# Kernel tuning notes

Hardware: AMD Instinct MI355X
Metric: run time of the kernel (lower is better)

The kernel has to match this reference:

```python
import jax, jax.numpy as jnp
import numpy as np

NOISE_EPS = 1e-2


def setup_inputs() -> dict:
    key = jax.random.key(0)
    ks = jax.random.split(key, 6)
    N, D, E, H = 16384, 512, 8, 1024
    x = jax.random.normal(ks[0], (N, D), jnp.float32)
    eps = jax.random.normal(ks[1], (N, E), jnp.float32)
    w_gate = jax.random.normal(ks[2], (D, E), jnp.float32) * 0.02
    w_noise = jax.random.normal(ks[3], (D, E), jnp.float32) * 0.02
    W_h = jnp.eye(E, dtype=jnp.float32)  # module initializes W_h = eye(num_experts)
    W1 = jax.random.normal(ks[4], (E, D, H), jnp.float32) * 0.02
    b1 = jnp.zeros((E, H), jnp.float32)
    W2 = jax.random.normal(ks[5], (E, H, D), jnp.float32) * 0.02
    b2 = jnp.zeros((E, D), jnp.float32)
    return dict(x=x, eps=eps, w_gate=w_gate, w_noise=w_noise, W_h=W_h,
                W1=W1, b1=b1, W2=W2, b2=b2, k=2, capacity=5120)


def reference(x, eps, w_gate, w_noise, W_h, W1, b1, W2, b2, k, capacity):
    N, D = x.shape
    E = w_gate.shape[1]
    # --- noisy top-k gating ---
    clean_logits = (x @ w_gate) @ W_h                       # [N, E]
    noise_stddev = jax.nn.softplus(x @ w_noise) + NOISE_EPS  # [N, E]
    noisy_logits = clean_logits + eps * noise_stddev
    top_vals, top_idx = jax.lax.top_k(noisy_logits, k)       # [N, k]
    top_gates = jax.nn.softmax(top_vals, axis=-1)
    gates = jnp.zeros((N, E), x.dtype).at[jnp.arange(N)[:, None], top_idx].set(top_gates)
    # --- capacity masking: keep the first `capacity` routed tokens per expert (batch order) ---
    active = gates > 0
    rank = jnp.cumsum(active, axis=0) - 1                    # per-expert arrival rank
    keep = active & (rank < capacity)
    gates = jnp.where(keep, gates, jnp.zeros((), x.dtype))
    # --- dispatch into fixed [E, capacity] buffers (dummy slot absorbs dropped writes) ---
    flat = jnp.where(keep, jnp.arange(E)[None, :] * capacity + rank, E * capacity)  # [N, E]
    tok = jnp.broadcast_to(jnp.arange(N, dtype=jnp.int32)[:, None], (N, E))
    buf = jnp.zeros(E * capacity + 1, jnp.int32).at[flat].set(tok)[:E * capacity].reshape(E, capacity)
    gbuf = jnp.zeros(E * capacity + 1, x.dtype).at[flat].set(gates)[:E * capacity].reshape(E, capacity)
    x_exp = x[buf]                                           # [E, C, D] gather
    # --- per-expert 1-layer FFN (grouped GEMM) ---
    h = jax.nn.relu(jnp.einsum('ecd,edh->ech', x_exp, W1) + b1[:, None, :])
    y_exp = jnp.einsum('ech,eho->eco', h, W2) + b2[:, None, :]
    # --- weighted scatter-combine (unfilled slots have gate 0, so they add nothing) ---
    weighted = y_exp * gbuf[..., None]
    combined = jnp.zeros((N, D), x.dtype).at[buf.reshape(-1)].add(weighted.reshape(-1, D))
    return combined
```

## Files before the change

kernel.cpp:

```cpp
#include <hip/hip_runtime.h>
#include <hip/hip_bf16.h>
#include <cstdint>

#define NTOK 16384
#define DIM 512
#define NEXP 8
#define HID 1024
#define CAPACITY 5120

typedef __attribute__((ext_vector_type(8))) short bf16x8;
typedef __attribute__((ext_vector_type(4))) float f32x4;
typedef unsigned long long u64;

__device__ __forceinline__ unsigned short f2bf(float f) {
    unsigned u = __float_as_uint(f);
    unsigned r = (u + 0x7FFFu + ((u >> 16) & 1u)) >> 16;
    return (unsigned short)r;
}

#define GLDS16(gp, lp) __builtin_amdgcn_global_load_lds( \
    (const __attribute__((address_space(1))) void*)(gp), \
    (__attribute__((address_space(3))) void*)(lp), 16, 0, 0)

__global__ __launch_bounds__(256) void gating_kernel(
    const float* __restrict__ x, const float* __restrict__ eps,
    const float* __restrict__ wg, const float* __restrict__ wn,
    const float* __restrict__ Wh, int2* __restrict__ rec)
{
    int w = threadIdx.x >> 6, lane = threadIdx.x & 63;
    int n = blockIdx.x * 4 + w;
    float ag[8], an[8];
#pragma unroll
    for (int e = 0; e < 8; ++e) { ag[e] = 0.f; an[e] = 0.f; }
    const float* xr = x + (size_t)n * DIM;
#pragma unroll
    for (int i = 0; i < DIM / 64; ++i) {
        int d = i * 64 + lane;
        float xv = xr[d];
        const float4* g4 = reinterpret_cast<const float4*>(wg + (size_t)d * 8);
        const float4* n4 = reinterpret_cast<const float4*>(wn + (size_t)d * 8);
        float4 a0 = g4[0], a1 = g4[1], b0 = n4[0], b1v = n4[1];
        ag[0] += xv * a0.x; ag[1] += xv * a0.y; ag[2] += xv * a0.z; ag[3] += xv * a0.w;
        ag[4] += xv * a1.x; ag[5] += xv * a1.y; ag[6] += xv * a1.z; ag[7] += xv * a1.w;
        an[0] += xv * b0.x; an[1] += xv * b0.y; an[2] += xv * b0.z; an[3] += xv * b0.w;
        an[4] += xv * b1v.x; an[5] += xv * b1v.y; an[6] += xv * b1v.z; an[7] += xv * b1v.w;
    }
#pragma unroll
    for (int off = 32; off; off >>= 1) {
#pragma unroll
        for (int e = 0; e < 8; ++e) {
            ag[e] += __shfl_xor(ag[e], off);
            an[e] += __shfl_xor(an[e], off);
        }
    }
    float noisy[8];
#pragma unroll
    for (int e = 0; e < 8; ++e) {
        float c = 0.f;
#pragma unroll
        for (int j = 0; j < 8; ++j) c += ag[j] * Wh[j * 8 + e];
        float v = an[e];
        float sp = fmaxf(v, 0.f) + log1pf(expf(-fabsf(v)));
        noisy[e] = c + eps[(size_t)n * 8 + e] * (sp + 1e-2f);
    }
    int i1 = 0; float v1 = noisy[0];
#pragma unroll
    for (int e = 1; e < 8; ++e) if (noisy[e] > v1) { v1 = noisy[e]; i1 = e; }
    int i2 = -1; float v2 = -3.4e38f;
#pragma unroll
    for (int e = 0; e < 8; ++e) if (e != i1 && noisy[e] > v2) { v2 = noisy[e]; i2 = e; }
    float ex = expf(v2 - v1);
    float g1 = 1.f / (1.f + ex);
    if (lane == 0)
        rec[n] = make_int2(i1 | (i2 << 8), __float_as_int(g1));
}

__global__ __launch_bounds__(1024) void scan_local(
    const int2* __restrict__ rec, unsigned* __restrict__ lrank, int* __restrict__ btot)
{
    __shared__ u64 wtot[16];
    __shared__ int wprefix[16][8];
    int tid = threadIdx.x, w = tid >> 6, lane = tid & 63;
    int n = blockIdx.x * 1024 + tid;
    int2 r = rec[n];
    int e1 = r.x & 0xFF, e2 = (r.x >> 8) & 0xFF;
    u64 m = (1ULL << (e1 * 8)) | (1ULL << (e2 * 8));
    u64 incl = m;
#pragma unroll
    for (int off = 1; off < 64; off <<= 1) {
        u64 v = __shfl_up(incl, off);
        if (lane >= off) incl += v;
    }
    if (lane == 63) wtot[w] = incl;
    __syncthreads();
    if (tid < 128) {
        int e = tid & 7, ww = tid >> 3;
        int s = 0;
        for (int j = 0; j < ww; ++j) s += (int)((wtot[j] >> (e * 8)) & 0xFF);
        wprefix[ww][e] = s;
        if (ww == 15)
            btot[blockIdx.x * 8 + e] = s + (int)((wtot[15] >> (e * 8)) & 0xFF);
    }
    __syncthreads();
    u64 excl = incl - m;
    unsigned l1 = (unsigned)(wprefix[w][e1] + (int)((excl >> (e1 * 8)) & 0xFF));
    unsigned l2 = (unsigned)(wprefix[w][e2] + (int)((excl >> (e2 * 8)) & 0xFF));
    lrank[n] = l1 | (l2 << 16);
}

__global__ __launch_bounds__(64) void scan_offs(
    const int* __restrict__ btot, int* __restrict__ off, int* __restrict__ counts,
    const int* __restrict__ cap_p)
{
    int e = threadIdx.x;
    if (e >= 8) return;
    int cap = *cap_p; if (cap > CAPACITY) cap = CAPACITY;
    int run = 0;
    for (int b = 0; b < 16; ++b) {
        off[b * 8 + e] = run;
        run += btot[b * 8 + e];
    }
    counts[e] = min(run, cap);
}

__global__ __launch_bounds__(1024) void scatter_k(
    const int2* __restrict__ rec, const unsigned* __restrict__ lrank,
    const int* __restrict__ off, const int* __restrict__ cap_p,
    int* __restrict__ buf, float* __restrict__ gbuf)
{
    int tid = threadIdx.x, b = blockIdx.x;
    int n = b * 1024 + tid;
    int cap = *cap_p; if (cap > CAPACITY) cap = CAPACITY;
    int2 r = rec[n];
    int e1 = r.x & 0xFF, e2 = (r.x >> 8) & 0xFF;
    float g1 = __int_as_float(r.y), g2 = 1.f - g1;
    unsigned lr = lrank[n];
    int r1 = off[b * 8 + e1] + (int)(lr & 0xFFFF);
    int r2 = off[b * 8 + e2] + (int)(lr >> 16);
    if (r1 < cap) { buf[e1 * CAPACITY + r1] = n; gbuf[e1 * CAPACITY + r1] = g1; }
    if (r2 < cap) { buf[e2 * CAPACITY + r2] = n; gbuf[e2 * CAPACITY + r2] = g2; }
}

__global__ __launch_bounds__(256) void gather_x(
    const float* __restrict__ x, const int* __restrict__ buf,
    const int* __restrict__ counts, unsigned short* __restrict__ xe)
{
    int slot = blockIdx.x * 4 + (threadIdx.x >> 6);
    int lane = threadIdx.x & 63;
    int e = slot / CAPACITY, rr = slot - e * CAPACITY;
    int4 v = make_int4(0, 0, 0, 0);
    if (rr < counts[e]) {
        int tok = buf[slot];
        const float* src = x + (size_t)tok * DIM + lane * 8;
        float4 a = *reinterpret_cast<const float4*>(src);
        float4 b = *reinterpret_cast<const float4*>(src + 4);
        v.x = f2bf(a.x) | ((int)f2bf(a.y) << 16);
        v.y = f2bf(a.z) | ((int)f2bf(a.w) << 16);
        v.z = f2bf(b.x) | ((int)f2bf(b.y) << 16);
        v.w = f2bf(b.z) | ((int)f2bf(b.w) << 16);
    }
    *reinterpret_cast<int4*>(xe + (size_t)e * CAPACITY * DIM +
                             ((size_t)lane * CAPACITY + rr) * 8) = v;
}

__global__ __launch_bounds__(256) void tcvt(const float* __restrict__ in,
                                            unsigned short* __restrict__ out, int R, int C)
{
    __shared__ float tile[32][33];
    int z = blockIdx.z;
    int c0 = blockIdx.x * 32, r0 = blockIdx.y * 32;
    int tx = threadIdx.x, ty = threadIdx.y;
    const float* inz = in + (size_t)z * R * C;
    unsigned short* outz = out + (size_t)z * R * C;
#pragma unroll
    for (int j = 0; j < 32; j += 8)
        tile[ty + j][tx] = inz[(size_t)(r0 + ty + j) * C + c0 + tx];
    __syncthreads();
#pragma unroll
    for (int j = 0; j < 32; j += 8)
        outz[(size_t)(c0 + ty + j) * R + r0 + tx] = f2bf(tile[tx][ty + j]);
}


#define STAGEB(T, BI)                                                      \
  {                                                                        \
    size_t k0_ = (size_t)(T) * 64;                                         \
    char* db_ = lds + (BI) * 16384 + w * 4096 + lane * 16;                 \
    GLDS16(Bt + boff[0] + k0_, db_);                                       \
    GLDS16(Bt + boff[1] + k0_, db_ + 1024);                                \
    GLDS16(Bt + boff[2] + k0_, db_ + 2048);                                \
    GLDS16(Bt + boff[3] + k0_, db_ + 3072);                                \
  }

#define LOADA(T, AF)                                                       \
  {                                                                        \
    const unsigned short* ab_ = A + abase + (size_t)(T) * (CAPACITY * 64); \
    _Pragma("unroll")                                                      \
    for (int kk = 0; kk < 2; ++kk)                                         \
      _Pragma("unroll")                                                    \
      for (int mi = 0; mi < 4; ++mi)                                       \
        AF[kk][mi] = *reinterpret_cast<const bf16x8*>(ab_ + voff[kk][mi]); \
  }

#define COMPUTE(BI, AF)                                                    \
  {                                                                        \
    const char* cb_ = lds + (BI) * 16384;                                  \
    _Pragma("unroll")                                                      \
    for (int kk = 0; kk < 2; ++kk) {                                       \
      bf16x8 bfr_[4];                                                      \
      _Pragma("unroll")                                                    \
      for (int ni = 0; ni < 4; ++ni) {                                     \
        int row_ = wn * 64 + ni * 16 + rl;                                 \
        int cc_ = (kk * 4 + q) ^ (row_ & 7);                               \
        bfr_[ni] = *reinterpret_cast<const bf16x8*>(cb_ + row_ * 128 + cc_ * 16); \
      }                                                                    \
      _Pragma("unroll")                                                    \
      for (int mi = 0; mi < 4; ++mi)                                       \
        _Pragma("unroll")                                                  \
        for (int ni = 0; ni < 4; ++ni)                                     \
          acc[mi][ni] = __builtin_amdgcn_mfma_f32_16x16x32_bf16(           \
              AF[kk][mi], bfr_[ni], acc[mi][ni], 0, 0, 0);                 \
    }                                                                      \
  }

#define VMCNT12 asm volatile("s_waitcnt vmcnt(12)" ::: "memory")
#define BARRIER asm volatile("s_barrier" ::: "memory")

template <int MODE>
__global__ __launch_bounds__(256) void ffn_gemm(
    const unsigned short* __restrict__ A, const unsigned short* __restrict__ Bt,
    const float* __restrict__ bias, unsigned short* __restrict__ Hout,
    float* __restrict__ Out, const int* __restrict__ buf,
    const float* __restrict__ gbuf, const int* __restrict__ counts,
    int Ka, int Nd)
{
    int flat = blockIdx.x + gridDim.x * (blockIdx.y + gridDim.y * blockIdx.z);
    int e  = flat & 7;
    int rr = flat >> 3;
    int tn = rr % gridDim.y;
    int tm = rr / gridDim.y;

    int cnt = counts[e];
    if (tm * 128 >= cnt) return;
    int tid = threadIdx.x, w = tid >> 6, lane = tid & 63;
    int q = lane >> 4, rl = lane & 15;
    int wm = w >> 1, wn = w & 1;

    __shared__ __align__(16) char lds[32768];

    unsigned boff[4];
#pragma unroll
    for (int i = 0; i < 4; ++i) {
        int p = (w * 4 + i) * 64 + lane;
        int row = p >> 3, kp = p & 7;
        int c = kp ^ (row & 7);
        boff[i] = (unsigned)(e * Nd + tn * 128 + row) * Ka + c * 8;
    }

    size_t abase = (size_t)e * CAPACITY * Ka;
    unsigned voff[2][4];
#pragma unroll
    for (int kk = 0; kk < 2; ++kk)
#pragma unroll
        for (int mi = 0; mi < 4; ++mi) {
            int row = tm * 128 + wm * 64 + mi * 16 + rl;
            voff[kk][mi] = (unsigned)((kk * 4 + q) * CAPACITY + row) * 8;
        }

    f32x4 acc[4][4];
#pragma unroll
    for (int mi = 0; mi < 4; ++mi)
#pragma unroll
        for (int ni = 0; ni < 4; ++ni)
            acc[mi][ni] = (f32x4){0.f, 0.f, 0.f, 0.f};

    int nk = Ka >> 6;

    bf16x8 afA[2][4], afB[2][4];

    STAGEB(0, 0);
    LOADA(0, afA);

    for (int t = 0; t < nk; t += 2) {
        {
            int tp = (t + 1 < nk) ? t + 1 : nk - 1;
            STAGEB(tp, (t + 1) & 1);
            LOADA(tp, afB);
            VMCNT12; BARRIER;
            COMPUTE(t & 1, afA);
            BARRIER;
        }
        {
            int tp = (t + 2 < nk) ? t + 2 : nk - 1;
            STAGEB(tp, (t + 2) & 1);
            LOADA(tp, afA);
            VMCNT12; BARRIER;
            COMPUTE((t + 1) & 1, afB);
            BARRIER;
        }
    }

    if (MODE == 1) {
        unsigned short* hb = Hout + (size_t)e * CAPACITY * HID;
#pragma unroll
        for (int ni = 0; ni < 4; ++ni) {
            int gcol = tn * 128 + wn * 64 + ni * 16 + rl;
            float bv = bias[e * Nd + gcol];
            size_t cb = ((size_t)(gcol >> 3) * CAPACITY) * 8 + (gcol & 7);
#pragma unroll
            for (int mi = 0; mi < 4; ++mi) {
#pragma unroll
                for (int r = 0; r < 4; ++r) {
                    int grow = tm * 128 + wm * 64 + mi * 16 + q * 4 + r;
                    float v = fmaxf(acc[mi][ni][r] + bv, 0.f);
                    hb[cb + (size_t)grow * 8] = f2bf(v);
                }
            }
        }
    } else {
        int ebase = e * CAPACITY;
#pragma unroll
        for (int ni = 0; ni < 4; ++ni) {
            int gcol = tn * 128 + wn * 64 + ni * 16 + rl;
            float bv = bias[e * Nd + gcol];
#pragma unroll
            for (int mi = 0; mi < 4; ++mi) {
#pragma unroll
                for (int r = 0; r < 4; ++r) {
                    int grow = tm * 128 + wm * 64 + mi * 16 + q * 4 + r;
                    if (grow < cnt) {
                        int tok = buf[ebase + grow];
                        float g = gbuf[ebase + grow];
                        float v = (acc[mi][ni][r] + bv) * g;
                        atomicAdd(Out + (size_t)tok * DIM + gcol, v);
                    }
                }
            }
        }
    }
}

extern "C" void kernel_launch(void* const* d_in, const int* in_sizes, int n_in,
                              void* d_out, int out_size, void* d_ws, size_t ws_size,
                              hipStream_t stream)
{
    const float* x   = (const float*)d_in[0];
    const float* eps = (const float*)d_in[1];
    const float* wg  = (const float*)d_in[2];
    const float* wn  = (const float*)d_in[3];
    const float* Wh  = (const float*)d_in[4];
    const float* W1  = (const float*)d_in[5];
    const float* b1  = (const float*)d_in[6];
    const float* W2  = (const float*)d_in[7];
    const float* b2  = (const float*)d_in[8];
    const int* capp  = (const int*)d_in[10];

    char* ws = (char*)d_ws;
    unsigned short* xe   = (unsigned short*)(ws);
    unsigned short* w1t  = (unsigned short*)(ws + 41943040);
    unsigned short* w2t  = (unsigned short*)(ws + 50331648);
    unsigned short* hK   = (unsigned short*)(ws + 58720256);
    int*      buf    = (int*)     (ws + 142606336);
    float*    gbuf   = (float*)   (ws + 142770176);
    int2*     rec    = (int2*)    (ws + 142934016);
    unsigned* lrank  = (unsigned*)(ws + 143065088);
    int*      btot   = (int*)     (ws + 143130624);
    int*      off    = (int*)     (ws + 143131136);
    int*      counts = (int*)     (ws + 143131648);

    float* out = (float*)d_out;
    hipMemsetAsync(out, 0, (size_t)out_size * sizeof(float), stream);

    gating_kernel<<<NTOK / 4, 256, 0, stream>>>(x, eps, wg, wn, Wh, rec);
    scan_local<<<16, 1024, 0, stream>>>(rec, lrank, btot);
    scan_offs<<<1, 64, 0, stream>>>(btot, off, counts, capp);
    scatter_k<<<16, 1024, 0, stream>>>(rec, lrank, off, capp, buf, gbuf);
    tcvt<<<dim3(HID / 32, DIM / 32, NEXP), dim3(32, 8), 0, stream>>>(W1, w1t, DIM, HID);
    tcvt<<<dim3(DIM / 32, HID / 32, NEXP), dim3(32, 8), 0, stream>>>(W2, w2t, HID, DIM);
    gather_x<<<NEXP * CAPACITY / 4, 256, 0, stream>>>(x, buf, counts, xe);

    ffn_gemm<1><<<dim3(CAPACITY / 128, HID / 128, NEXP), 256, 0, stream>>>(
        xe, w1t, b1, hK, nullptr, buf, gbuf, counts, DIM, HID);
    ffn_gemm<0><<<dim3(CAPACITY / 128, DIM / 128, NEXP), 256, 0, stream>>>(
        hK, w2t, b2, nullptr, out, buf, gbuf, counts, HID, DIM);
}
```

Measured before the change: 273.4 us.

## Rewrite expert GEMM as 256x256 tiles with LDS-staged A and 8-phase pipeline

Changes the expert FFN GEMM from 128x128 tiles on 256 threads to 256x256 tiles on 512 threads, with 128 KB of double-buffered LDS. Both A and B are now staged through LDS via global_load_lds, where before A fragments were loaded straight into registers. The K loop is split into eight phases that interleave half-tile loads with MFMA bursts under setprio and sched barriers. The gather and hidden-output layouts switch from k-interleaved to plain row-major to match. The aim is higher operand reuse per tile and better overlap of memory traffic with MFMA work, at the cost of fewer blocks (ceil(count/256) per expert), more register pressure and more padded tail work.

```diff
diff --git a/kernel.cpp b/kernel.cpp
--- a/kernel.cpp
+++ b/kernel.cpp
@@ -146,12 +146,12 @@
     const int* __restrict__ counts, unsigned short* __restrict__ xe)
 {
     int slot = blockIdx.x * 4 + (threadIdx.x >> 6);
-    int lane = threadIdx.x & 63;
+    int d0 = (threadIdx.x & 63) * 8;
     int e = slot / CAPACITY, rr = slot - e * CAPACITY;
     int4 v = make_int4(0, 0, 0, 0);
     if (rr < counts[e]) {
         int tok = buf[slot];
-        const float* src = x + (size_t)tok * DIM + lane * 8;
+        const float* src = x + (size_t)tok * DIM + d0;
         float4 a = *reinterpret_cast<const float4*>(src);
         float4 b = *reinterpret_cast<const float4*>(src + 4);
         v.x = f2bf(a.x) | ((int)f2bf(a.y) << 16);
@@ -159,8 +159,7 @@
         v.z = f2bf(b.x) | ((int)f2bf(b.y) << 16);
         v.w = f2bf(b.z) | ((int)f2bf(b.w) << 16);
     }
-    *reinterpret_cast<int4*>(xe + (size_t)e * CAPACITY * DIM +
-                             ((size_t)lane * CAPACITY + rr) * 8) = v;
+    *reinterpret_cast<int4*>(xe + (size_t)slot * DIM + d0) = v;
 }
 
 __global__ __launch_bounds__(256) void tcvt(const float* __restrict__ in,
@@ -182,52 +181,59 @@
 }
 
 
-#define STAGEB(T, BI)                                                      \
-  {                                                                        \
-    size_t k0_ = (size_t)(T) * 64;                                         \
-    char* db_ = lds + (BI) * 16384 + w * 4096 + lane * 16;                 \
-    GLDS16(Bt + boff[0] + k0_, db_);                                       \
-    GLDS16(Bt + boff[1] + k0_, db_ + 1024);                                \
-    GLDS16(Bt + boff[2] + k0_, db_ + 2048);                                \
-    GLDS16(Bt + boff[3] + k0_, db_ + 3072);                                \
+#define STG(T, OPB, H)                                                          \
+  {                                                                             \
+    int dp_ = ((T) & 1);                                                        \
+    int tc_ = ((T) < nk) ? (T) : (nk - 1);                                      \
+    size_t k0_ = (size_t)tc_ * 64;                                              \
+    char* d_ = lds + dp_ * 65536 + (OPB) * 32768 + (H) * 16384 + tid * 16;      \
+    if ((OPB) == 0) {                                                           \
+      GLDS16(A + asrc[H][0] + k0_, d_);                                         \
+      GLDS16(A + asrc[H][1] + k0_, d_ + 8192);                                  \
+    } else {                                                                    \
+      GLDS16(Bt + bsrc[H][0] + k0_, d_);                                        \
+      GLDS16(Bt + bsrc[H][1] + k0_, d_ + 8192);                                 \
+    }                                                                           \
   }
 
-#define LOADA(T, AF)                                                       \
-  {                                                                        \
-    const unsigned short* ab_ = A + abase + (size_t)(T) * (CAPACITY * 64); \
-    _Pragma("unroll")                                                      \
-    for (int kk = 0; kk < 2; ++kk)                                         \
-      _Pragma("unroll")                                                    \
-      for (int mi = 0; mi < 4; ++mi)                                       \
-        AF[kk][mi] = *reinterpret_cast<const bf16x8*>(ab_ + voff[kk][mi]); \
+#define PH(P, ST_T, ST_OP, ST_H)                                                \
+  {                                                                             \
+    STG(ST_T, ST_OP, ST_H);                                                     \
+    if constexpr ((P) == 0 || (P) == 4)                                         \
+      asm volatile("s_waitcnt vmcnt(2)" ::: "memory");                          \
+    __builtin_amdgcn_s_barrier();                                               \
+    const char* cb_ = lds + (((P) >= 4) ? 65536 : 0);                           \
+    constexpr int kk_ = ((P) >> 1) & 1;                                         \
+    constexpr int np_ = (P) & 1;                                                \
+    if constexpr (((P) & 1) == 0) {                                             \
+      _Pragma("unroll")                                                         \
+      for (int mi = 0; mi < 8; ++mi)                                            \
+        af[mi] = *reinterpret_cast<const bf16x8*>(                              \
+            cb_ + wm * 16384 + ((mi * 16 + rl) << 7) + (cc[kk_] << 4));         \
+    }                                                                           \
+    bf16x8 bfr_[2];                                                             \
+    _Pragma("unroll")                                                           \
+    for (int nl = 0; nl < 2; ++nl) {                                            \
+      int row_ = brl + (np_ * 2 + nl) * 16 + rl;                                \
+      bfr_[nl] = *reinterpret_cast<const bf16x8*>(                              \
+          cb_ + 32768 + bh * 16384 + (row_ << 7) + (cc[kk_] << 4));             \
+    }                                                                           \
+    asm volatile("s_waitcnt lgkmcnt(0)" ::: "memory");                          \
+    __builtin_amdgcn_sched_barrier(0);                                          \
+    __builtin_amdgcn_s_setprio(1);                                              \
+    _Pragma("unroll")                                                           \
+    for (int mi = 0; mi < 8; ++mi)                                              \
+      _Pragma("unroll")                                                         \
+      for (int nl = 0; nl < 2; ++nl)                                            \
+        acc[mi][np_ * 2 + nl] = __builtin_amdgcn_mfma_f32_16x16x32_bf16(        \
+            af[mi], bfr_[nl], acc[mi][np_ * 2 + nl], 0, 0, 0);                  \
+    __builtin_amdgcn_s_setprio(0);                                              \
+    __builtin_amdgcn_sched_barrier(0);                                          \
+    __builtin_amdgcn_s_barrier();                                               \
   }
 
-#define COMPUTE(BI, AF)                                                    \
-  {                                                                        \
-    const char* cb_ = lds + (BI) * 16384;                                  \
-    _Pragma("unroll")                                                      \
-    for (int kk = 0; kk < 2; ++kk) {                                       \
-      bf16x8 bfr_[4];                                                      \
-      _Pragma("unroll")                                                    \
-      for (int ni = 0; ni < 4; ++ni) {                                     \
-        int row_ = wn * 64 + ni * 16 + rl;                                 \
-        int cc_ = (kk * 4 + q) ^ (row_ & 7);                               \
-        bfr_[ni] = *reinterpret_cast<const bf16x8*>(cb_ + row_ * 128 + cc_ * 16); \
-      }                                                                    \
-      _Pragma("unroll")                                                    \
-      for (int mi = 0; mi < 4; ++mi)                                       \
-        _Pragma("unroll")                                                  \
-        for (int ni = 0; ni < 4; ++ni)                                     \
-          acc[mi][ni] = __builtin_amdgcn_mfma_f32_16x16x32_bf16(           \
-              AF[kk][mi], bfr_[ni], acc[mi][ni], 0, 0, 0);                 \
-    }                                                                      \
-  }
-
-#define VMCNT12 asm volatile("s_waitcnt vmcnt(12)" ::: "memory")
-#define BARRIER asm volatile("s_barrier" ::: "memory")
-
 template <int MODE>
-__global__ __launch_bounds__(256) void ffn_gemm(
+__global__ __launch_bounds__(512, 2) void ffn_gemm(
     const unsigned short* __restrict__ A, const unsigned short* __restrict__ Bt,
     const float* __restrict__ bias, unsigned short* __restrict__ Hout,
     float* __restrict__ Out, const int* __restrict__ buf,
@@ -241,79 +247,66 @@
     int tm = rr / gridDim.y;
 
     int cnt = counts[e];
-    if (tm * 128 >= cnt) return;
+    if (tm * 256 >= cnt) return;
     int tid = threadIdx.x, w = tid >> 6, lane = tid & 63;
     int q = lane >> 4, rl = lane & 15;
-    int wm = w >> 1, wn = w & 1;
-
-    __shared__ __align__(16) char lds[32768];
-
-    unsigned boff[4];
-#pragma unroll
-    for (int i = 0; i < 4; ++i) {
-        int p = (w * 4 + i) * 64 + lane;
-        int row = p >> 3, kp = p & 7;
-        int c = kp ^ (row & 7);
-        boff[i] = (unsigned)(e * Nd + tn * 128 + row) * Ka + c * 8;
-    }
-
-    size_t abase = (size_t)e * CAPACITY * Ka;
-    unsigned voff[2][4];
-#pragma unroll
-    for (int kk = 0; kk < 2; ++kk)
-#pragma unroll
-        for (int mi = 0; mi < 4; ++mi) {
-            int row = tm * 128 + wm * 64 + mi * 16 + rl;
-            voff[kk][mi] = (unsigned)((kk * 4 + q) * CAPACITY + row) * 8;
+    int wm = w >> 2, wn = w & 3;
+    int bh = wn >> 1, brl = (wn & 1) * 64;
+
+    __shared__ __align__(16) char lds[131072];
+
+    int cc[2] = { q ^ (rl & 7), (4 + q) ^ (rl & 7) };
+
+    size_t asrc[2][2], bsrc[2][2];
+#pragma unroll
+    for (int h = 0; h < 2; ++h)
+#pragma unroll
+        for (int j = 0; j < 2; ++j) {
+            int row = (tid + j * 512) >> 3;
+            int kc = tid & 7;
+            int kcs = kc ^ (row & 7);
+            asrc[h][j] = (size_t)(e * CAPACITY + tm * 256 + h * 128 + row) * Ka + kcs * 8;
+            bsrc[h][j] = (size_t)(e * Nd + tn * 256 + h * 128 + row) * Ka + kcs * 8;
         }
 
-    f32x4 acc[4][4];
-#pragma unroll
-    for (int mi = 0; mi < 4; ++mi)
+    f32x4 acc[8][4];
+#pragma unroll
+    for (int mi = 0; mi < 8; ++mi)
 #pragma unroll
         for (int ni = 0; ni < 4; ++ni)
             acc[mi][ni] = (f32x4){0.f, 0.f, 0.f, 0.f};
 
     int nk = Ka >> 6;
-
-    bf16x8 afA[2][4], afB[2][4];
-
-    STAGEB(0, 0);
-    LOADA(0, afA);
-
-    for (int t = 0; t < nk; t += 2) {
-        {
-            int tp = (t + 1 < nk) ? t + 1 : nk - 1;
-            STAGEB(tp, (t + 1) & 1);
-            LOADA(tp, afB);
-            VMCNT12; BARRIER;
-            COMPUTE(t & 1, afA);
-            BARRIER;
-        }
-        {
-            int tp = (t + 2 < nk) ? t + 2 : nk - 1;
-            STAGEB(tp, (t + 2) & 1);
-            LOADA(tp, afA);
-            VMCNT12; BARRIER;
-            COMPUTE((t + 1) & 1, afB);
-            BARRIER;
-        }
+    int niter = nk >> 1;
+
+    bf16x8 af[8];
+
+    STG(0, 0, 0); STG(0, 0, 1); STG(0, 1, 0); STG(0, 1, 1);
+
+    for (int i = 0; i < niter; ++i) {
+        int u = 2 * i;
+        PH(0, u + 1, 0, 0);
+        PH(1, u + 1, 0, 1);
+        PH(2, u + 1, 1, 0);
+        PH(3, u + 1, 1, 1);
+        PH(4, u + 2, 0, 0);
+        PH(5, u + 2, 0, 1);
+        PH(6, u + 2, 1, 0);
+        PH(7, u + 2, 1, 1);
     }
 
     if (MODE == 1) {
-        unsigned short* hb = Hout + (size_t)e * CAPACITY * HID;
 #pragma unroll
         for (int ni = 0; ni < 4; ++ni) {
-            int gcol = tn * 128 + wn * 64 + ni * 16 + rl;
+            int gcol = tn * 256 + wn * 64 + ni * 16 + rl;
             float bv = bias[e * Nd + gcol];
-            size_t cb = ((size_t)(gcol >> 3) * CAPACITY) * 8 + (gcol & 7);
-#pragma unroll
-            for (int mi = 0; mi < 4; ++mi) {
+#pragma unroll
+            for (int mi = 0; mi < 8; ++mi) {
 #pragma unroll
                 for (int r = 0; r < 4; ++r) {
-                    int grow = tm * 128 + wm * 64 + mi * 16 + q * 4 + r;
+                    int grow = tm * 256 + wm * 128 + mi * 16 + q * 4 + r;
                     float v = fmaxf(acc[mi][ni][r] + bv, 0.f);
-                    hb[cb + (size_t)grow * 8] = f2bf(v);
+                    Hout[(size_t)(e * CAPACITY + grow) * HID + gcol] = f2bf(v);
                 }
             }
         }
@@ -321,13 +314,13 @@
         int ebase = e * CAPACITY;
 #pragma unroll
         for (int ni = 0; ni < 4; ++ni) {
-            int gcol = tn * 128 + wn * 64 + ni * 16 + rl;
+            int gcol = tn * 256 + wn * 64 + ni * 16 + rl;
             float bv = bias[e * Nd + gcol];
 #pragma unroll
-            for (int mi = 0; mi < 4; ++mi) {
+            for (int mi = 0; mi < 8; ++mi) {
 #pragma unroll
                 for (int r = 0; r < 4; ++r) {
-                    int grow = tm * 128 + wm * 64 + mi * 16 + q * 4 + r;
+                    int grow = tm * 256 + wm * 128 + mi * 16 + q * 4 + r;
                     if (grow < cnt) {
                         int tok = buf[ebase + grow];
                         float g = gbuf[ebase + grow];
@@ -379,8 +372,8 @@
     tcvt<<<dim3(DIM / 32, HID / 32, NEXP), dim3(32, 8), 0, stream>>>(W2, w2t, HID, DIM);
     gather_x<<<NEXP * CAPACITY / 4, 256, 0, stream>>>(x, buf, counts, xe);
 
-    ffn_gemm<1><<<dim3(CAPACITY / 128, HID / 128, NEXP), 256, 0, stream>>>(
+    ffn_gemm<1><<<dim3(CAPACITY / 256, HID / 256, NEXP), 512, 0, stream>>>(
         xe, w1t, b1, hK, nullptr, buf, gbuf, counts, DIM, HID);
-    ffn_gemm<0><<<dim3(CAPACITY / 128, DIM / 128, NEXP), 256, 0, stream>>>(
+    ffn_gemm<0><<<dim3(CAPACITY / 256, DIM / 256, NEXP), 512, 0, stream>>>(
         hK, w2t, b2, nullptr, out, buf, gbuf, counts, HID, DIM);
 }
```

Measured after the change: 294.1 us. +7.6%, slower.
